# Performance work log

Hardware: AMD Instinct MI355X
Metric: run time of the kernel (lower is better)

Reference implementation:

```python
import jax, jax.numpy as jnp
import numpy as np

E, FF, H, PE = 256, 1024, 8, 32

def _ln(x, g, b, eps=1e-5):
    m = jnp.mean(x, axis=-1, keepdims=True)
    v = jnp.var(x, axis=-1, keepdims=True)
    return (x - m) / jnp.sqrt(v + eps) * g + b

def setup_inputs() -> dict:
    key = jax.random.key(0)
    ks = jax.random.split(key, 24)
    B, N, NH = 2, 8192, 8
    w = lambda i, shape: (jax.random.normal(ks[i], shape, jnp.float32) * 0.02)
    return {
        'x': jax.random.normal(ks[0], (B, N, NH, E), jnp.float32),
        'pos1': jax.random.normal(ks[1], (B, N, NH, 2), jnp.float32),
        'pos2': jax.random.normal(ks[2], (B, N, NH, 2), jnp.float32),
        'W_in': w(3, (E, E)), 'g_in': jnp.ones((E,), jnp.float32), 'b_in': jnp.zeros((E,), jnp.float32),
        'Wq': w(4, (E, E)), 'bq': jnp.zeros((E,), jnp.float32),
        'Wk': w(5, (E, E)), 'bk': jnp.zeros((E,), jnp.float32),
        'Wv': w(6, (E, E)), 'bv': jnp.zeros((E,), jnp.float32),
        'Wo': w(7, (E, E)), 'bo': jnp.zeros((E,), jnp.float32),
        'W_pos': w(8, (4, PE)), 'W_bias': w(9, (PE, H)),
        'W_ff1': w(10, (E, FF)), 'W_ff2': w(11, (FF, E)),
        'g1': jnp.ones((E,), jnp.float32), 'b1': jnp.zeros((E,), jnp.float32),
        'g2': jnp.ones((E,), jnp.float32), 'b2': jnp.zeros((E,), jnp.float32),
    }

def reference(x, pos1, pos2, W_in, g_in, b_in, Wq, bq, Wk, bk, Wv, bv, Wo, bo,
              W_pos, W_bias, W_ff1, W_ff2, g1, b1, g2, b2):
    B, N, NH, e = x.shape
    d = e // H
    # input_mlp: Linear(no bias) + LayerNorm
    t = _ln(x @ W_in, g_in, b_in).reshape(B * N, NH, e)  # (BN, nh, E); q=k=v=t
    q = (t @ Wq + bq).reshape(B * N, NH, H, d)
    k = (t @ Wk + bk).reshape(B * N, NH, H, d)
    v = (t @ Wv + bv).reshape(B * N, NH, H, d)
    scores = jnp.einsum('bqhd,bkhd->bhqk', q, k) / jnp.sqrt(jnp.float32(d))  # (BN,H,nh,nh)
    # positional bias: pos_embedder(pos1,pos2) -> emb_proj_bias -> per-key per-head bias
    emb = jax.nn.silu(jnp.concatenate([pos1, pos2], axis=-1) @ W_pos)  # (B,N,nh,PE)
    bias = (emb @ W_bias).reshape(B * N, NH, H)  # (BN, nh_key, H)
    scores = scores + jnp.transpose(bias, (0, 2, 1))[:, :, None, :]  # broadcast over queries
    att = jax.nn.softmax(scores, axis=-1)
    att_out = jnp.einsum('bhqk,bkhd->bqhd', att, v).reshape(B * N, NH, e)
    att_out = att_out @ Wo + bo
    h1 = _ln(t + att_out, g1, b1)  # q_res residual on pre-projection q
    h2 = _ln(h1 + jax.nn.silu(h1 @ W_ff1) @ W_ff2, g2, b2)
    return h2.reshape(B, N, NH, e)
```

## Files before the change

kernel.cpp:

```cpp
#include <hip/hip_runtime.h>
#include <cstdint>
#include <cstddef>

typedef unsigned short ushort_t;
typedef __attribute__((ext_vector_type(8))) short short8;
typedef __attribute__((ext_vector_type(4))) short short4v;
typedef __attribute__((ext_vector_type(4))) float floatx4;

__device__ __forceinline__ float b2f(ushort_t u) {
    unsigned v = ((unsigned)u) << 16;
    return __builtin_bit_cast(float, v);
}
__device__ __forceinline__ float b2fs(short s) { return b2f((ushort_t)s); }
__device__ __forceinline__ ushort_t f2b(float f) {
    unsigned u = __builtin_bit_cast(unsigned, f);
    u += 0x7fffu + ((u >> 16) & 1u);
    return (ushort_t)(u >> 16);
}

__device__ __forceinline__ void load_lds16(const ushort_t* g, ushort_t* l) {
    __builtin_amdgcn_global_load_lds(
        (const __attribute__((address_space(1))) void*)g,
        (__attribute__((address_space(3))) void*)l, 16, 0, 0);
}

template <int NT, bool A_F32, bool HAS_BIAS, bool DO_SILU>
__global__ __launch_bounds__(256, 2) void gemm_strip(
    const void* __restrict__ Ap, const ushort_t* __restrict__ BT,
    const float* __restrict__ bias, ushort_t* __restrict__ out)
{
    constexpr int K = 256;
    constexpr int ldN = NT * 128;
    __shared__ __align__(16) ushort_t As[128 * 256];
    __shared__ __align__(16) ushort_t Bs[128 * 64];

    const int tid = threadIdx.x;
    const int w = tid >> 6, lane = tid & 63;
    const int wm = w >> 1, wn = w & 1;
    const int quad = lane >> 4, r = lane & 15;
    const size_t m0 = (size_t)blockIdx.x * 128;

    if (A_F32) {
        const float* A = (const float*)Ap;
#pragma unroll
        for (int it = 0; it < 16; ++it) {
            int c = it * 256 + tid;
            int row = c >> 5, col = (c & 31) * 8;
            const float* p = A + (m0 + row) * K + col;
            float4 a = *(const float4*)p;
            float4 b = *(const float4*)(p + 4);
            short8 o;
            o[0] = (short)f2b(a.x); o[1] = (short)f2b(a.y);
            o[2] = (short)f2b(a.z); o[3] = (short)f2b(a.w);
            o[4] = (short)f2b(b.x); o[5] = (short)f2b(b.y);
            o[6] = (short)f2b(b.z); o[7] = (short)f2b(b.w);
            *(short8*)(As + row * 256 + col) = o;
        }
    } else {
        const ushort_t* A = (const ushort_t*)Ap;
#pragma unroll
        for (int it = 0; it < 16; ++it) {
            int row = it * 8 + w * 2 + (lane >> 5);
            load_lds16(A + (m0 + row) * K + (lane & 31) * 8,
                       As + (it * 8 + w * 2) * 256);
        }
    }

    for (int nt_i = 0; nt_i < NT; ++nt_i) {
        const int n0 = nt_i * 128;
        floatx4 acc[4][4];
#pragma unroll
        for (int nt = 0; nt < 4; ++nt)
#pragma unroll
            for (int mt = 0; mt < 4; ++mt)
#pragma unroll
                for (int rg = 0; rg < 4; ++rg) acc[nt][mt][rg] = 0.f;

#pragma unroll
        for (int kc = 0; kc < 4; ++kc) {
            __syncthreads();
#pragma unroll
            for (int i = 0; i < 4; ++i) {
                int row = i * 32 + w * 8 + (lane >> 3);
                load_lds16(BT + (size_t)(n0 + row) * K + kc * 64 + (lane & 7) * 8,
                           Bs + (i * 32 + w * 8) * 64);
            }
            __syncthreads();
#pragma unroll
            for (int ks = 0; ks < 2; ++ks) {
                short8 af[4];
#pragma unroll
                for (int mt = 0; mt < 4; ++mt)
                    af[mt] = *(const short8*)(As + (wm * 64 + mt * 16 + r) * 256
                                              + kc * 64 + ks * 32 + quad * 8);
#pragma unroll
                for (int nt = 0; nt < 4; ++nt) {
                    short8 bf_ = *(const short8*)(Bs + (wn * 64 + nt * 16 + r) * 64
                                                  + ks * 32 + quad * 8);
#pragma unroll
                    for (int mt = 0; mt < 4; ++mt)
                        acc[nt][mt] = __builtin_amdgcn_mfma_f32_16x16x32_bf16(
                            af[mt], bf_, acc[nt][mt], 0, 0, 0);
                }
            }
        }
#pragma unroll
        for (int nt = 0; nt < 4; ++nt) {
            int col = n0 + wn * 64 + nt * 16 + r;
            float bv = 0.f;
            if (HAS_BIAS) bv = bias[col];
#pragma unroll
            for (int mt = 0; mt < 4; ++mt) {
#pragma unroll
                for (int rg = 0; rg < 4; ++rg) {
                    size_t row = m0 + wm * 64 + mt * 16 + quad * 4 + rg;
                    float v = acc[nt][mt][rg] + bv;
                    if (DO_SILU) v = v / (1.f + __expf(-v));
                    out[row * ldN + col] = f2b(v);
                }
            }
        }
    }
}

__global__ __launch_bounds__(256, 2) void gemm_wide(
    const ushort_t* __restrict__ A, const ushort_t* __restrict__ BT,
    ushort_t* __restrict__ out)
{
    constexpr int K = 1024, N = 256;
    __shared__ __align__(16) ushort_t As[128 * 64];
    __shared__ __align__(16) ushort_t Bs[256 * 64];

    const int tid = threadIdx.x;
    const int w = tid >> 6, lane = tid & 63;
    const int wm = w >> 1, wn = w & 1;
    const int quad = lane >> 4, r = lane & 15;
    const size_t m0 = (size_t)blockIdx.x * 128;

    floatx4 acc[8][4];
#pragma unroll
    for (int nt = 0; nt < 8; ++nt)
#pragma unroll
        for (int mt = 0; mt < 4; ++mt)
#pragma unroll
            for (int rg = 0; rg < 4; ++rg) acc[nt][mt][rg] = 0.f;

    for (int kc = 0; kc < K / 64; ++kc) {
        __syncthreads();
#pragma unroll
        for (int i = 0; i < 4; ++i) {
            int row = i * 32 + w * 8 + (lane >> 3);
            load_lds16(A + (m0 + row) * K + kc * 64 + (lane & 7) * 8,
                       As + (i * 32 + w * 8) * 64);
        }
#pragma unroll
        for (int i = 0; i < 8; ++i) {
            int row = i * 32 + w * 8 + (lane >> 3);
            load_lds16(BT + (size_t)row * K + kc * 64 + (lane & 7) * 8,
                       Bs + (i * 32 + w * 8) * 64);
        }
        __syncthreads();
#pragma unroll
        for (int ks = 0; ks < 2; ++ks) {
            short8 af[4];
#pragma unroll
            for (int mt = 0; mt < 4; ++mt)
                af[mt] = *(const short8*)(As + (wm * 64 + mt * 16 + r) * 64
                                          + ks * 32 + quad * 8);
#pragma unroll
            for (int nt = 0; nt < 8; ++nt) {
                short8 bf_ = *(const short8*)(Bs + (wn * 128 + nt * 16 + r) * 64
                                              + ks * 32 + quad * 8);
#pragma unroll
                for (int mt = 0; mt < 4; ++mt)
                    acc[nt][mt] = __builtin_amdgcn_mfma_f32_16x16x32_bf16(
                        af[mt], bf_, acc[nt][mt], 0, 0, 0);
            }
        }
    }
#pragma unroll
    for (int nt = 0; nt < 8; ++nt) {
        int col = wn * 128 + nt * 16 + r;
#pragma unroll
        for (int mt = 0; mt < 4; ++mt)
#pragma unroll
            for (int rg = 0; rg < 4; ++rg) {
                size_t row = m0 + wm * 64 + mt * 16 + quad * 4 + rg;
                out[row * N + col] = f2b(acc[nt][mt][rg]);
            }
    }
}

template <bool OUT_F32>
__global__ __launch_bounds__(256) void ln_kernel(
    const ushort_t* __restrict__ y, const ushort_t* __restrict__ res,
    const float* __restrict__ g, const float* __restrict__ b,
    void* __restrict__ outv)
{
    const int w = threadIdx.x >> 6;
    const int lane = threadIdx.x & 63;
    const size_t row = (size_t)blockIdx.x * 4 + w;
    const size_t base = row * 256 + lane * 4;

    short4v vy = *(const short4v*)(y + base);
    float v[4];
#pragma unroll
    for (int j = 0; j < 4; ++j) v[j] = b2fs(vy[j]);
    if (res) {
        short4v vr = *(const short4v*)(res + base);
#pragma unroll
        for (int j = 0; j < 4; ++j) v[j] += b2fs(vr[j]);
    }
    float s = v[0] + v[1] + v[2] + v[3];
    float sq = v[0] * v[0] + v[1] * v[1] + v[2] * v[2] + v[3] * v[3];
#pragma unroll
    for (int off = 32; off > 0; off >>= 1) {
        s += __shfl_xor(s, off, 64);
        sq += __shfl_xor(sq, off, 64);
    }
    float mean = s * (1.f / 256.f);
    float var = sq * (1.f / 256.f) - mean * mean;
    float rstd = rsqrtf(var + 1e-5f);
    if (OUT_F32) {
        float4 ov;
        int col = lane * 4;
        ov.x = (v[0] - mean) * rstd * g[col + 0] + b[col + 0];
        ov.y = (v[1] - mean) * rstd * g[col + 1] + b[col + 1];
        ov.z = (v[2] - mean) * rstd * g[col + 2] + b[col + 2];
        ov.w = (v[3] - mean) * rstd * g[col + 3] + b[col + 3];
        *(float4*)((float*)outv + base) = ov;
    } else {
        short4v ov;
#pragma unroll
        for (int j = 0; j < 4; ++j) {
            int col = lane * 4 + j;
            float o = (v[j] - mean) * rstd * g[col] + b[col];
            ov[j] = (short)f2b(o);
        }
        *(short4v*)((ushort_t*)outv + base) = ov;
    }
}

__global__ __launch_bounds__(256) void attn_kernel(
    const ushort_t* __restrict__ qkv,
    const float* __restrict__ pos1, const float* __restrict__ pos2,
    const float* __restrict__ Wpos, const float* __restrict__ Wbias,
    ushort_t* __restrict__ att_out)
{
    __shared__ __align__(16) ushort_t qkv_s[4][8 * 768];
    __shared__ float bias_s[4][8][8];
    __shared__ float wpos_s[128];
    __shared__ float wbias_s[256];

    const int tid = threadIdx.x;
    if (tid < 128) wpos_s[tid] = Wpos[tid];
    wbias_s[tid] = Wbias[tid];

    const int w = tid >> 6;
    const int lane = tid & 63;
    const int tok = blockIdx.x * 4 + w;

    const ushort_t* src = qkv + (size_t)tok * 8 * 768;
    for (int c = lane; c < 768; c += 64)
        *(short8*)(qkv_s[w] + c * 8) = *(const short8*)(src + c * 8);
    __syncthreads();

    {
        const int j = lane >> 3, h = lane & 7;
        const size_t pbase = ((size_t)tok * 8 + j) * 2;
        float p0 = pos1[pbase], p1 = pos1[pbase + 1];
        float p2 = pos2[pbase], p3 = pos2[pbase + 1];
        float acc = 0.f;
#pragma unroll
        for (int p = 0; p < 32; ++p) {
            float e = p0 * wpos_s[p] + p1 * wpos_s[32 + p] + p2 * wpos_s[64 + p] + p3 * wpos_s[96 + p];
            e = e / (1.f + __expf(-e));
            acc += e * wbias_s[p * 8 + h];
        }
        bias_s[w][j][h] = acc;
    }
    __syncthreads();

    const int i = lane >> 3, h = lane & 7;
    const ushort_t* qrow = qkv_s[w] + i * 768 + h * 32;
    float q[32];
#pragma unroll
    for (int c = 0; c < 4; ++c) {
        short8 t8 = *(const short8*)(qrow + c * 8);
#pragma unroll
        for (int e = 0; e < 8; ++e) q[c * 8 + e] = b2fs(t8[e]);
    }
    float s[8];
#pragma unroll
    for (int jj = 0; jj < 8; ++jj) {
        const ushort_t* krow = qkv_s[w] + jj * 768 + 256 + h * 32;
        float d = 0.f;
#pragma unroll
        for (int c = 0; c < 4; ++c) {
            short8 t8 = *(const short8*)(krow + c * 8);
#pragma unroll
            for (int e = 0; e < 8; ++e) d += q[c * 8 + e] * b2fs(t8[e]);
        }
        s[jj] = d * 0.17677669529663688f + bias_s[w][jj][h];
    }
    float mx = s[0];
#pragma unroll
    for (int jj = 1; jj < 8; ++jj) mx = fmaxf(mx, s[jj]);
    float l = 0.f;
#pragma unroll
    for (int jj = 0; jj < 8; ++jj) { s[jj] = __expf(s[jj] - mx); l += s[jj]; }
    float rl = 1.f / l;
    float o[32];
#pragma unroll
    for (int e = 0; e < 32; ++e) o[e] = 0.f;
#pragma unroll
    for (int jj = 0; jj < 8; ++jj) {
        float p = s[jj] * rl;
        const ushort_t* vrow = qkv_s[w] + jj * 768 + 512 + h * 32;
#pragma unroll
        for (int c = 0; c < 4; ++c) {
            short8 t8 = *(const short8*)(vrow + c * 8);
#pragma unroll
            for (int e = 0; e < 8; ++e) o[c * 8 + e] += p * b2fs(t8[e]);
        }
    }
    ushort_t* orow = att_out + ((size_t)tok * 8 + i) * 256 + h * 32;
#pragma unroll
    for (int c = 0; c < 4; ++c) {
        short8 t8;
#pragma unroll
        for (int e = 0; e < 8; ++e) t8[e] = (short)f2b(o[c * 8 + e]);
        *(short8*)(orow + c * 8) = t8;
    }
}

__global__ void transpose_kernel(const float* __restrict__ in,
                                 ushort_t* __restrict__ out, int K, int N)
{
    int idx = blockIdx.x * 256 + threadIdx.x;
    if (idx < K * N) {
        int k = idx / N, n = idx % N;
        out[n * K + k] = f2b(in[idx]);
    }
}

__global__ void pack_bias_kernel(const float* a, const float* b,
                                 const float* c, float* out)
{
    int t = blockIdx.x * 256 + threadIdx.x;
    if (t < 256) out[t] = a[t];
    else if (t < 512) out[t] = b[t - 256];
    else if (t < 768) out[t] = c[t - 512];
}

extern "C" void kernel_launch(void* const* d_in, const int* in_sizes, int n_in,
                              void* d_out, int out_size, void* d_ws, size_t ws_size,
                              hipStream_t stream)
{
    const float* x     = (const float*)d_in[0];
    const float* pos1  = (const float*)d_in[1];
    const float* pos2  = (const float*)d_in[2];
    const float* W_in  = (const float*)d_in[3];
    const float* g_in  = (const float*)d_in[4];
    const float* b_in  = (const float*)d_in[5];
    const float* Wq    = (const float*)d_in[6];
    const float* bq    = (const float*)d_in[7];
    const float* Wk    = (const float*)d_in[8];
    const float* bk    = (const float*)d_in[9];
    const float* Wv    = (const float*)d_in[10];
    const float* bv    = (const float*)d_in[11];
    const float* Wo    = (const float*)d_in[12];
    const float* bo    = (const float*)d_in[13];
    const float* W_pos = (const float*)d_in[14];
    const float* W_bias= (const float*)d_in[15];
    const float* W_ff1 = (const float*)d_in[16];
    const float* W_ff2 = (const float*)d_in[17];
    const float* g1    = (const float*)d_in[18];
    const float* b1    = (const float*)d_in[19];
    const float* g2    = (const float*)d_in[20];
    const float* b2    = (const float*)d_in[21];

    const int M = in_sizes[0] / 256;
    const int ntok = M / 8;

    ushort_t* ws    = (ushort_t*)d_ws;
    ushort_t* WinT  = ws;
    ushort_t* WqkvT = ws + 65536;
    ushort_t* WoT   = ws + 262144;
    ushort_t* Wff1T = ws + 327680;
    ushort_t* Wff2T = ws + 589824;
    float*    bqkv  = (float*)(ws + 851968);
    ushort_t* bufA  = (ushort_t*)((char*)d_ws + (2ull << 20));
    ushort_t* bufB  = bufA + (size_t)M * 256;
    ushort_t* bufC  = bufB + (size_t)M * 256;

    transpose_kernel<<<256, 256, 0, stream>>>(W_in, WinT, 256, 256);
    transpose_kernel<<<256, 256, 0, stream>>>(Wq, WqkvT, 256, 256);
    transpose_kernel<<<256, 256, 0, stream>>>(Wk, WqkvT + 65536, 256, 256);
    transpose_kernel<<<256, 256, 0, stream>>>(Wv, WqkvT + 131072, 256, 256);
    transpose_kernel<<<256, 256, 0, stream>>>(Wo, WoT, 256, 256);
    transpose_kernel<<<1024, 256, 0, stream>>>(W_ff1, Wff1T, 256, 1024);
    transpose_kernel<<<1024, 256, 0, stream>>>(W_ff2, Wff2T, 1024, 256);
    pack_bias_kernel<<<3, 256, 0, stream>>>(bq, bk, bv, bqkv);

    dim3 blk(256);
    gemm_strip<2, true, false, false><<<M / 128, blk, 0, stream>>>(x, WinT, nullptr, bufA);
    ln_kernel<false><<<M / 4, blk, 0, stream>>>(bufA, nullptr, g_in, b_in, bufB);
    gemm_strip<6, false, true, false><<<M / 128, blk, 0, stream>>>(bufB, WqkvT, bqkv, bufC);
    attn_kernel<<<ntok / 4, blk, 0, stream>>>(bufC, pos1, pos2, W_pos, W_bias, bufA);
    gemm_strip<2, false, true, false><<<M / 128, blk, 0, stream>>>(bufA, WoT, bo, bufC);
    ln_kernel<false><<<M / 4, blk, 0, stream>>>(bufC, bufB, g1, b1, bufA);
    gemm_strip<8, false, false, true><<<M / 128, blk, 0, stream>>>(bufA, Wff1T, nullptr, bufC);
    gemm_wide<<<M / 128, blk, 0, stream>>>(bufC, Wff2T, bufB);
    ln_kernel<true><<<M / 4, blk, 0, stream>>>(bufB, bufA, g2, b2, d_out);
}
```

Baseline: 1.014 ms.

## Hold A fragments in registers and XOR-swizzle LDS tiles in GEMM kernels

The strip GEMM now loads each wave's A rows straight from global memory into registers (32 short8 fragments) instead of staging the whole 128x256 A tile in LDS. The freed LDS holds a full-K 128x256 B tile per output strip, which cuts the syncs per strip from eight to two. Both the strip and wide GEMMs use an XOR swizzle on the LDS column slot to reduce bank conflicts on fragment reads. The cost is much higher VGPR pressure (128 registers for A alone), which may reduce occupancy or cause spills under launch_bounds(256,2), and A global loads are now row-strided per lane rather than coalesced.

```diff
diff --git a/kernel.cpp b/kernel.cpp
--- a/kernel.cpp
+++ b/kernel.cpp
@@ -25,14 +25,13 @@
 }
 
 template <int NT, bool A_F32, bool HAS_BIAS, bool DO_SILU>
-__global__ __launch_bounds__(256, 2) void gemm_strip(
+__global__ __launch_bounds__(256, 2) void gemm_areg(
     const void* __restrict__ Ap, const ushort_t* __restrict__ BT,
     const float* __restrict__ bias, ushort_t* __restrict__ out)
 {
     constexpr int K = 256;
     constexpr int ldN = NT * 128;
-    __shared__ __align__(16) ushort_t As[128 * 256];
-    __shared__ __align__(16) ushort_t Bs[128 * 64];
+    __shared__ __align__(16) ushort_t Bs[128 * 256];
 
     const int tid = threadIdx.x;
     const int w = tid >> 6, lane = tid & 63;
@@ -40,34 +39,50 @@
     const int quad = lane >> 4, r = lane & 15;
     const size_t m0 = (size_t)blockIdx.x * 128;
 
+    short8 af[4][8];
     if (A_F32) {
         const float* A = (const float*)Ap;
 #pragma unroll
-        for (int it = 0; it < 16; ++it) {
-            int c = it * 256 + tid;
-            int row = c >> 5, col = (c & 31) * 8;
-            const float* p = A + (m0 + row) * K + col;
-            float4 a = *(const float4*)p;
-            float4 b = *(const float4*)(p + 4);
-            short8 o;
-            o[0] = (short)f2b(a.x); o[1] = (short)f2b(a.y);
-            o[2] = (short)f2b(a.z); o[3] = (short)f2b(a.w);
-            o[4] = (short)f2b(b.x); o[5] = (short)f2b(b.y);
-            o[6] = (short)f2b(b.z); o[7] = (short)f2b(b.w);
-            *(short8*)(As + row * 256 + col) = o;
+        for (int mt = 0; mt < 4; ++mt) {
+            const float* rp = A + (m0 + wm * 64 + mt * 16 + r) * K + quad * 8;
+#pragma unroll
+            for (int kk = 0; kk < 8; ++kk) {
+                float4 a = *(const float4*)(rp + kk * 32);
+                float4 b = *(const float4*)(rp + kk * 32 + 4);
+                short8 o;
+                o[0] = (short)f2b(a.x); o[1] = (short)f2b(a.y);
+                o[2] = (short)f2b(a.z); o[3] = (short)f2b(a.w);
+                o[4] = (short)f2b(b.x); o[5] = (short)f2b(b.y);
+                o[6] = (short)f2b(b.z); o[7] = (short)f2b(b.w);
+                af[mt][kk] = o;
+            }
         }
     } else {
         const ushort_t* A = (const ushort_t*)Ap;
 #pragma unroll
-        for (int it = 0; it < 16; ++it) {
-            int row = it * 8 + w * 2 + (lane >> 5);
-            load_lds16(A + (m0 + row) * K + (lane & 31) * 8,
-                       As + (it * 8 + w * 2) * 256);
-        }
-    }
+        for (int mt = 0; mt < 4; ++mt) {
+            const ushort_t* rp = A + (m0 + wm * 64 + mt * 16 + r) * K + quad * 8;
+#pragma unroll
+            for (int kk = 0; kk < 8; ++kk)
+                af[mt][kk] = *(const short8*)(rp + kk * 32);
+        }
+    }
+
+    const int srow_off = w * 2 + (lane >> 5);
+    const int sslot = (lane & 31) ^ (srow_off & 7);
+    const int rsw = (r & 7) << 3;
 
     for (int nt_i = 0; nt_i < NT; ++nt_i) {
         const int n0 = nt_i * 128;
+        __syncthreads();
+#pragma unroll
+        for (int i = 0; i < 16; ++i) {
+            int row = i * 8 + srow_off;
+            load_lds16(BT + (size_t)(n0 + row) * K + sslot * 8,
+                       Bs + (i * 8 + w * 2) * 256);
+        }
+        __syncthreads();
+
         floatx4 acc[4][4];
 #pragma unroll
         for (int nt = 0; nt < 4; ++nt)
@@ -77,31 +92,16 @@
                 for (int rg = 0; rg < 4; ++rg) acc[nt][mt][rg] = 0.f;
 
 #pragma unroll
-        for (int kc = 0; kc < 4; ++kc) {
-            __syncthreads();
-#pragma unroll
-            for (int i = 0; i < 4; ++i) {
-                int row = i * 32 + w * 8 + (lane >> 3);
-                load_lds16(BT + (size_t)(n0 + row) * K + kc * 64 + (lane & 7) * 8,
-                           Bs + (i * 32 + w * 8) * 64);
-            }
-            __syncthreads();
-#pragma unroll
-            for (int ks = 0; ks < 2; ++ks) {
-                short8 af[4];
+        for (int kk = 0; kk < 8; ++kk) {
+            const int koff = (kk * 32 + quad * 8) ^ rsw;
+#pragma unroll
+            for (int nt = 0; nt < 4; ++nt) {
+                int col = wn * 64 + nt * 16 + r;
+                short8 bf_ = *(const short8*)(Bs + col * 256 + koff);
 #pragma unroll
                 for (int mt = 0; mt < 4; ++mt)
-                    af[mt] = *(const short8*)(As + (wm * 64 + mt * 16 + r) * 256
-                                              + kc * 64 + ks * 32 + quad * 8);
-#pragma unroll
-                for (int nt = 0; nt < 4; ++nt) {
-                    short8 bf_ = *(const short8*)(Bs + (wn * 64 + nt * 16 + r) * 64
-                                                  + ks * 32 + quad * 8);
-#pragma unroll
-                    for (int mt = 0; mt < 4; ++mt)
-                        acc[nt][mt] = __builtin_amdgcn_mfma_f32_16x16x32_bf16(
-                            af[mt], bf_, acc[nt][mt], 0, 0, 0);
-                }
+                    acc[nt][mt] = __builtin_amdgcn_mfma_f32_16x16x32_bf16(
+                        af[mt][kk], bf_, acc[nt][mt], 0, 0, 0);
             }
         }
 #pragma unroll
@@ -137,6 +137,9 @@
     const int quad = lane >> 4, r = lane & 15;
     const size_t m0 = (size_t)blockIdx.x * 128;
 
+    const int sslot8 = (lane & 7) ^ ((lane >> 3) & 7);
+    const int rsw = (r & 7) << 3;
+
     floatx4 acc[8][4];
 #pragma unroll
     for (int nt = 0; nt < 8; ++nt)
@@ -150,27 +153,26 @@
 #pragma unroll
         for (int i = 0; i < 4; ++i) {
             int row = i * 32 + w * 8 + (lane >> 3);
-            load_lds16(A + (m0 + row) * K + kc * 64 + (lane & 7) * 8,
+            load_lds16(A + (m0 + row) * K + kc * 64 + sslot8 * 8,
                        As + (i * 32 + w * 8) * 64);
         }
 #pragma unroll
         for (int i = 0; i < 8; ++i) {
             int row = i * 32 + w * 8 + (lane >> 3);
-            load_lds16(BT + (size_t)row * K + kc * 64 + (lane & 7) * 8,
+            load_lds16(BT + (size_t)row * K + kc * 64 + sslot8 * 8,
                        Bs + (i * 32 + w * 8) * 64);
         }
         __syncthreads();
 #pragma unroll
         for (int ks = 0; ks < 2; ++ks) {
+            const int koff = (ks * 32 + quad * 8) ^ rsw;
             short8 af[4];
 #pragma unroll
             for (int mt = 0; mt < 4; ++mt)
-                af[mt] = *(const short8*)(As + (wm * 64 + mt * 16 + r) * 64
-                                          + ks * 32 + quad * 8);
+                af[mt] = *(const short8*)(As + (wm * 64 + mt * 16 + r) * 64 + koff);
 #pragma unroll
             for (int nt = 0; nt < 8; ++nt) {
-                short8 bf_ = *(const short8*)(Bs + (wn * 128 + nt * 16 + r) * 64
-                                              + ks * 32 + quad * 8);
+                short8 bf_ = *(const short8*)(Bs + (wn * 128 + nt * 16 + r) * 64 + koff);
 #pragma unroll
                 for (int mt = 0; mt < 4; ++mt)
                     acc[nt][mt] = __builtin_amdgcn_mfma_f32_16x16x32_bf16(
@@ -404,13 +406,13 @@
     pack_bias_kernel<<<3, 256, 0, stream>>>(bq, bk, bv, bqkv);
 
     dim3 blk(256);
-    gemm_strip<2, true, false, false><<<M / 128, blk, 0, stream>>>(x, WinT, nullptr, bufA);
+    gemm_areg<2, true, false, false><<<M / 128, blk, 0, stream>>>(x, WinT, nullptr, bufA);
     ln_kernel<false><<<M / 4, blk, 0, stream>>>(bufA, nullptr, g_in, b_in, bufB);
-    gemm_strip<6, false, true, false><<<M / 128, blk, 0, stream>>>(bufB, WqkvT, bqkv, bufC);
+    gemm_areg<6, false, true, false><<<M / 128, blk, 0, stream>>>(bufB, WqkvT, bqkv, bufC);
     attn_kernel<<<ntok / 4, blk, 0, stream>>>(bufC, pos1, pos2, W_pos, W_bias, bufA);
-    gemm_strip<2, false, true, false><<<M / 128, blk, 0, stream>>>(bufA, WoT, bo, bufC);
+    gemm_areg<2, false, true, false><<<M / 128, blk, 0, stream>>>(bufA, WoT, bo, bufC);
     ln_kernel<false><<<M / 4, blk, 0, stream>>>(bufC, bufB, g1, b1, bufA);
-    gemm_strip<8, false, false, true><<<M / 128, blk, 0, stream>>>(bufA, Wff1T, nullptr, bufC);
+    gemm_areg<8, false, false, true><<<M / 128, blk, 0, stream>>>(bufA, Wff1T, nullptr, bufC);
     gemm_wide<<<M / 128, blk, 0, stream>>>(bufC, Wff2T, bufB);
     ln_kernel<true><<<M / 4, blk, 0, stream>>>(bufB, bufA, g2, b2, d_out);
 }
```

Result: faster. 914.6 us (-9.8%).
